# Optimization experiments

Hardware: AMD Instinct MI355X
Metric: run time of the kernel (lower is better)

Reference implementation:

```python
import jax, jax.numpy as jnp
import numpy as np

N, F, HID, OUT, H = 4096, 128, 64, 16, 4
ALPHA = 0.2          # leaky relu slope
NEG = -9e15          # mask fill value (pyGAT convention)


def setup_inputs() -> dict:
    key = jax.random.key(0)
    ks = jax.random.split(key, 8)
    x = jax.random.normal(ks[0], (N, F), dtype=jnp.float32)
    adj = jax.random.randint(ks[1], (N, N), 0, 2, dtype=jnp.int32)
    s = lambda *sh: 0.1
    W_in = jax.random.normal(ks[2], (H, F, F), dtype=jnp.float32) * 0.1
    a_in = jax.random.normal(ks[3], (H, 2 * F), dtype=jnp.float32) * 0.1
    W_hid = jax.random.normal(ks[4], (H, F * H, HID), dtype=jnp.float32) * 0.1
    a_hid = jax.random.normal(ks[5], (H, 2 * HID), dtype=jnp.float32) * 0.1
    W_out = jax.random.normal(ks[6], (HID * H, OUT), dtype=jnp.float32) * 0.1
    a_out = jax.random.normal(ks[7], (2 * OUT,), dtype=jnp.float32) * 0.1
    return {"x": x, "adj": adj, "W_in": W_in, "a_in": a_in,
            "W_hid": W_hid, "a_hid": a_hid, "W_out": W_out, "a_out": a_out}


def _multi_head_att(x, W, a, mask):
    """Dense multi-head GAT aggregation. x:[N,Fin], W:[H,Fin,D], a:[H,2D] -> [H,N,D]."""
    D = W.shape[-1]
    h = jnp.einsum('nf,hfd->hnd', x, W)                      # [H,N,D]
    f1 = jnp.einsum('hnd,hd->hn', h, a[:, :D])               # source scores
    f2 = jnp.einsum('hnd,hd->hn', h, a[:, D:])               # target scores
    e = jax.nn.leaky_relu(f1[:, :, None] + f2[:, None, :], ALPHA)  # [H,N,N]
    e = jnp.where(mask[None, :, :], e, NEG)
    att = jax.nn.softmax(e, axis=-1)
    return jnp.einsum('hnm,hmd->hnd', att, h)                # [H,N,D]


def _concat_heads(h):
    # [H,N,D] -> [N,H*D]
    Hh, n, d = h.shape
    return jnp.transpose(h, (1, 0, 2)).reshape(n, Hh * d)


def reference(x, adj, W_in, a_in, W_hid, a_hid, W_out, a_out):
    mask = adj > 0
    # input attention block: concat=True (ELU per head), identity skip (in==out dim)
    h1 = _multi_head_att(x, W_in, a_in, mask)                # [H,N,F]
    h1 = jax.nn.elu(h1 + x[None, :, :])                      # identity residual
    h1 = _concat_heads(h1)                                   # [N,H*F]
    # hidden attention block: concat=True
    h2 = _multi_head_att(h1, W_hid, a_hid, mask)             # [H,N,HID]
    h2 = _concat_heads(jax.nn.elu(h2))                       # [N,H*HID]
    # output attention layer: single head, concat=False (no ELU inside)
    h3 = _multi_head_att(h2, W_out[None], a_out[None], mask)[0]  # [N,OUT]
    return jax.nn.log_softmax(jax.nn.elu(h3), axis=1)
```

## Files before the change

### kernel.cpp

```cpp
#include <hip/hip_runtime.h>
#include <math.h>

#define NN 4096
#define FF 128
#define HH 4
#define HIDD 64
#define OUTD 16
#define MASKW (NN / 32)
#define ALPHA 0.2f

typedef __attribute__((ext_vector_type(8))) short short8;
typedef __attribute__((ext_vector_type(4))) float f32x4;

__device__ __forceinline__ ushort f2bf(float f) {
    unsigned u = __float_as_uint(f);
    return (ushort)((u + 0x7fffu + ((u >> 16) & 1u)) >> 16);
}
__device__ __forceinline__ float bf2f(ushort u) {
    return __uint_as_float((unsigned)u << 16);
}

__global__ void pack_mask_kernel(const int* __restrict__ adj, unsigned int* __restrict__ mb) {
    int t = blockIdx.x * 256 + threadIdx.x;
    int v = adj[t] > 0;
    unsigned long long bal = __ballot(v);
    if ((threadIdx.x & 63) == 0) {
        int w = t >> 5;
        mb[w] = (unsigned int)(bal & 0xffffffffULL);
        mb[w + 1] = (unsigned int)(bal >> 32);
    }
}

__global__ void cvt_kernel(const float* __restrict__ x, ushort* __restrict__ xb) {
    int e = (blockIdx.x * 256 + threadIdx.x) * 4;
    f32x4 v = *(const f32x4*)&x[e];
    unsigned lo = (unsigned)f2bf(v[0]) | ((unsigned)f2bf(v[1]) << 16);
    unsigned hi = (unsigned)f2bf(v[2]) | ((unsigned)f2bf(v[3]) << 16);
    uint2 p; p.x = lo; p.y = hi;
    *(uint2*)&xb[e] = p;
}

__global__ void wtprep_kernel(const float* __restrict__ W_in, const float* __restrict__ W_hid,
                              const float* __restrict__ W_out,
                              ushort* __restrict__ wt1, ushort* __restrict__ wt2,
                              ushort* __restrict__ wt3) {
    int idx = blockIdx.x * 256 + threadIdx.x;
    if (idx < 65536) {
        int k = idx & 127, n = (idx >> 7) & 127, hd = idx >> 14;
        wt1[idx] = f2bf(W_in[((size_t)hd * 128 + k) * 128 + n]);
    } else if (idx < 65536 + 131072) {
        int j = idx - 65536;
        int k = j & 511, n = (j >> 9) & 63, hd = j >> 15;
        wt2[j] = f2bf(W_hid[((size_t)hd * 512 + k) * 64 + n]);
    } else if (idx < 65536 + 131072 + 4096) {
        int j = idx - 196608;
        int k = j & 255, n = j >> 8;
        wt3[j] = f2bf(W_out[(size_t)k * 16 + n]);
    }
}

__global__ void vprep_kernel(const float* __restrict__ W_in, const float* __restrict__ a_in,
                             const float* __restrict__ W_hid, const float* __restrict__ a_hid,
                             const float* __restrict__ W_out, const float* __restrict__ a_out,
                             float* __restrict__ vbuf) {
    int idx = blockIdx.x * 256 + threadIdx.x;
    const float* Wr; const float* ar; int D; float* dst;
    if (idx < 1024) {
        int f = idx & 127, hd = (idx >> 7) & 3, s = idx >> 9;
        Wr = W_in + ((size_t)hd * 128 + f) * 128;
        ar = a_in + hd * 256 + s * 128;
        D = 128; dst = &vbuf[idx];
    } else if (idx < 1024 + 4096) {
        int j = idx - 1024;
        int f = j & 511, hd = (j >> 9) & 3, s = j >> 11;
        Wr = W_hid + ((size_t)hd * 512 + f) * 64;
        ar = a_hid + hd * 128 + s * 64;
        D = 64; dst = &vbuf[1024 + j];
    } else if (idx < 1024 + 4096 + 512) {
        int j = idx - 5120;
        int f = j & 255, s = j >> 8;
        Wr = W_out + (size_t)f * 16;
        ar = a_out + s * 16;
        D = 16; dst = &vbuf[5120 + j];
    } else return;
    float s = 0.f;
    for (int d = 0; d < D; d++) s += Wr[d] * ar[d];
    *dst = s;
}

template <typename T, int K, int H>
__global__ __launch_bounds__(256) void score_kernel(const T* __restrict__ A,
                                                    const float* __restrict__ v,
                                                    float* __restrict__ f1,
                                                    float* __restrict__ f2) {
    int wv = blockIdx.x * 4 + (threadIdx.x >> 6);
    int lane = threadIdx.x & 63;
    int hd = wv >> 12;
    int i = wv & (NN - 1);
    const T* ar = A + (size_t)i * K;
    const float* v1r = v + (size_t)hd * K;
    const float* v2r = v + (size_t)(H + hd) * K;
    float s1 = 0.f, s2 = 0.f;
    for (int f = lane; f < K; f += 64) {
        float av;
        if constexpr (sizeof(T) == 2) av = bf2f(((const ushort*)ar)[f]);
        else av = ((const float*)ar)[f];
        s1 += av * v1r[f];
        s2 += av * v2r[f];
    }
#pragma unroll
    for (int o = 32; o > 0; o >>= 1) {
        s1 += __shfl_down(s1, o);
        s2 += __shfl_down(s2, o);
    }
    if (lane == 0) { f1[wv] = s1; f2[wv] = s2; }
}

__global__ void gmax_kernel(const float* __restrict__ f2, float* __restrict__ gmax) {
    int hd = blockIdx.x;
    const float* p = f2 + (size_t)hd * NN;
    float m = -1e30f;
    for (int i = threadIdx.x; i < NN; i += 256) m = fmaxf(m, p[i]);
    __shared__ float sm[4];
#pragma unroll
    for (int off = 32; off > 0; off >>= 1) m = fmaxf(m, __shfl_down(m, off));
    if ((threadIdx.x & 63) == 0) sm[threadIdx.x >> 6] = m;
    __syncthreads();
    if (threadIdx.x == 0) gmax[hd] = fmaxf(fmaxf(sm[0], sm[1]), fmaxf(sm[2], sm[3]));
}

template <int K, int N, int CFG>
__global__ __launch_bounds__(256) void proj_mfma_kernel(const ushort* __restrict__ A,
                                                        const ushort* __restrict__ WT,
                                                        ushort* __restrict__ hT) {
    constexpr int NT = (CFG == 0) ? (N / 64) : (N / 16);
    __shared__ ushort ts[4][NT * 16][20];
    const int hd = blockIdx.y;
    const int t = threadIdx.x;
    const int w = t >> 6, lane = t & 63, ln = lane & 15, g = lane >> 4, g8 = g * 8;
    const int i0 = (CFG == 0) ? blockIdx.x * 16 : blockIdx.x * 64 + w * 16;
    const int n0 = (CFG == 0) ? w * (N / 4) : 0;
    const ushort* WTh = WT + (size_t)hd * N * K;
    ushort* hTh = hT + (size_t)hd * N * NN;
    f32x4 acc[NT];
#pragma unroll
    for (int n = 0; n < NT; n++) acc[n] = (f32x4)(0.f);
    const ushort* arow = A + (size_t)(i0 + ln) * K + g8;
#pragma unroll
    for (int k0 = 0; k0 < K; k0 += 32) {
        short8 aF = *(const short8*)&arow[k0];
#pragma unroll
        for (int n = 0; n < NT; n++) {
            short8 bF = *(const short8*)&WTh[(size_t)(n0 + n * 16 + ln) * K + k0 + g8];
            acc[n] = __builtin_amdgcn_mfma_f32_16x16x32_bf16(aF, bF, acc[n], 0, 0, 0);
        }
    }
#pragma unroll
    for (int n = 0; n < NT; n++) {
        unsigned lo = (unsigned)f2bf(acc[n][0]) | ((unsigned)f2bf(acc[n][1]) << 16);
        unsigned hi = (unsigned)f2bf(acc[n][2]) | ((unsigned)f2bf(acc[n][3]) << 16);
        uint2 p; p.x = lo; p.y = hi;
        *(uint2*)&ts[w][n * 16 + ln][g * 4] = p;
    }
#pragma unroll
    for (int n = 0; n < NT; n++) {
        int d = lane >> 2, ip = lane & 3;
        uint2 rv = *(uint2*)&ts[w][n * 16 + d][ip * 4];
        *(uint2*)&hTh[(size_t)(n0 + n * 16 + d) * NN + i0 + ip * 4] = rv;
    }
}

template <int D>
__global__ __launch_bounds__(256) void agg4_kernel(const ushort* __restrict__ hT,
                                                   const float* __restrict__ f1,
                                                   const float* __restrict__ f2,
                                                   const float* __restrict__ gmax,
                                                   const unsigned int* __restrict__ mb,
                                                   float* __restrict__ pacc,
                                                   float* __restrict__ plsum,
                                                   int lgJS) {
    constexpr int NT = D / 16;
    constexpr int CHS = NT * 64;
    constexpr int NC = NT / 2;
    __shared__ ushort hs[2 * CHS * 8];
    const int JS = 1 << lgJS;
    const int jlen = NN >> lgJS;
    const int combos = JS * HH;
    const int bid = blockIdx.x;
    int ibk, combo;
    if (combos >= 8) {
        int xcd = bid & 7;
        int sid = bid >> 3;
        combo = xcd * (combos >> 3) + (sid >> 6);
        ibk = sid & 63;
    } else {
        ibk = bid & 63;
        combo = bid >> 6;
    }
    const int js = combo & (JS - 1);
    const int hd = combo >> lgJS;
    const int jb = js * jlen, je = jb + jlen;

    const int t = threadIdx.x;
    const int w = t >> 6;
    const int lane = t & 63;
    const int ln = lane & 15;
    const int g = lane >> 4;
    const int g8 = g * 8;
    const int i0 = ibk * 64 + w * 16;
    const ushort* hTh = hT + (size_t)hd * D * NN;

    const float f1v = f1[hd * NN + i0 + ln];
    const float gm = gmax[hd];
    float mi = f1v + gm;
    mi = fmaxf(mi, ALPHA * mi);
    const float L2E = 1.442695040888963f;
    const float cexp = -mi * L2E;

    f32x4 acc[NT];
#pragma unroll
    for (int n = 0; n < NT; n++) acc[n] = (f32x4)(0.f);
    float lsum = 0.f;
    const float* f2h = f2 + hd * NN;
    const unsigned* mrow = mb + (size_t)(i0 + ln) * MASKW;

    int srow[NC], scol[NC], soff[NC];
#pragma unroll
    for (int c = 0; c < NC; c++) {
        int ch = t + c * 256;
        int s = ch / CHS;
        int inner = ch - s * CHS;
        int n = inner >> 6;
        int l = inner & 63;
        srow[c] = n * 16 + (l & 15);
        scol[c] = s * 32 + (l >> 4) * 8;
        soff[c] = ch * 8;
    }
    uint4 st[NC];
#pragma unroll
    for (int c = 0; c < NC; c++)
        st[c] = *(const uint4*)&hTh[(size_t)srow[c] * NN + jb + scol[c]];

    for (int j0 = jb; j0 < je; j0 += 64) {
        __syncthreads();
#pragma unroll
        for (int c = 0; c < NC; c++) *(uint4*)&hs[soff[c]] = st[c];
        __syncthreads();
        const bool more = (j0 + 64) < je;
        if (more) {
#pragma unroll
            for (int c = 0; c < NC; c++)
                st[c] = *(const uint4*)&hTh[(size_t)srow[c] * NN + j0 + 64 + scol[c]];
        }
        uint2 mw2 = *(const uint2*)&mrow[j0 >> 5];
#pragma unroll
        for (int s = 0; s < 2; s++) {
            unsigned bits = ((s ? mw2.y : mw2.x) >> g8) & 0xffu;
            f32x4 cA = *(const f32x4*)&f2h[j0 + s * 32 + g8];
            f32x4 cB = *(const f32x4*)&f2h[j0 + s * 32 + g8 + 4];
            unsigned au[4];
#pragma unroll
            for (int tp = 0; tp < 4; tp++) {
                unsigned pu[2];
#pragma unroll
                for (int q = 0; q < 2; q++) {
                    int tt = tp * 2 + q;
                    float f2t = (tt < 4) ? cA[tt] : cB[tt - 4];
                    float e = f1v + f2t;
                    e = fmaxf(e, ALPHA * e);
                    float p = ((bits >> tt) & 1u) ? __builtin_amdgcn_exp2f(e * L2E + cexp) : 0.f;
                    pu[q] = __float_as_uint(p) & 0xffff0000u;
                    lsum += __uint_as_float(pu[q]);
                }
                au[tp] = (pu[0] >> 16) | pu[1];
            }
            union { unsigned u[4]; short8 v; } aF;
#pragma unroll
            for (int q = 0; q < 4; q++) aF.u[q] = au[q];
#pragma unroll
            for (int n = 0; n < NT; n++) {
                short8 bF = *(const short8*)&hs[((s * NT + n) * 64 + lane) * 8];
                acc[n] = __builtin_amdgcn_mfma_f32_16x16x32_bf16(aF.v, bF, acc[n], 0, 0, 0);
            }
        }
    }
    lsum += __shfl_xor(lsum, 16);
    lsum += __shfl_xor(lsum, 32);
    if (g == 0) plsum[(size_t)combo * NN + i0 + ln] = lsum;
    float* pb = pacc + ((size_t)combo * NN + i0) * D;
#pragma unroll
    for (int n = 0; n < NT; n++) {
#pragma unroll
        for (int r = 0; r < 4; r++) {
            pb[n * 256 + (g * 4 + r) * 16 + ln] = acc[n][r];
        }
    }
}

template <int D, int EPI>
__global__ __launch_bounds__(256) void combine_kernel(const float* __restrict__ pacc,
                                                      const float* __restrict__ plsum,
                                                      const float* __restrict__ xres,
                                                      ushort* __restrict__ out,
                                                      int ncols, int JS) {
    const int hd = blockIdx.y;
    const int e = (blockIdx.x * 256 + threadIdx.x) * 4;
    const int row = e / D;
    const int col = e % D;
    const size_t fidx = ((size_t)(row & ~15)) * D + (col >> 4) * 256 + (row & 15) * 16 + (col & 15);
    f32x4 s = (f32x4)(0.f);
    float l = 0.f;
    for (int js = 0; js < JS; js++) {
        const size_t cix = (size_t)(hd * JS + js) * NN;
        s += *(const f32x4*)&pacc[cix * D + fidx];
        l += plsum[cix + row];
    }
    const float inv = 1.f / l;
    f32x4 xv;
    if (EPI == 1) xv = *(const f32x4*)&xres[(size_t)row * D + col];
    float o[4];
#pragma unroll
    for (int k = 0; k < 4; k++) {
        float v = s[k] * inv;
        if (EPI == 1) v += xv[k];
        if (EPI >= 1) v = v > 0.f ? v : (__expf(v) - 1.f);
        o[k] = v;
    }
    unsigned lo = (unsigned)f2bf(o[0]) | ((unsigned)f2bf(o[1]) << 16);
    unsigned hi = (unsigned)f2bf(o[2]) | ((unsigned)f2bf(o[3]) << 16);
    uint2 p; p.x = lo; p.y = hi;
    *(uint2*)&out[(size_t)row * ncols + hd * D + col] = p;
}

template <int D, int EPI>
__global__ __launch_bounds__(256) void agg2_kernel(const ushort* __restrict__ hT,
                                                   const float* __restrict__ f1,
                                                   const float* __restrict__ f2,
                                                   const float* __restrict__ gmax,
                                                   const unsigned int* __restrict__ mb,
                                                   const float* __restrict__ xres,
                                                   ushort* __restrict__ out, int ncols) {
    constexpr int NT = D / 16;
    constexpr int NC = D / 64;
    __shared__ ushort hs[D][40];
    const int hd = blockIdx.z;
    const int t = threadIdx.x;
    const int w = t >> 6;
    const int lane = t & 63;
    const int ln = lane & 15;
    const int g = lane >> 4;
    const int g8 = g * 8;
    const int i0 = blockIdx.x * 64 + w * 16;
    const ushort* hTh = hT + (size_t)hd * D * NN;
    const float f1v = f1[hd * NN + i0 + ln];
    const float gm = gmax[hd];
    float mi = f1v + gm;
    mi = fmaxf(mi, ALPHA * mi);
    const float L2E = 1.442695040888963f;
    const float cexp = -mi * L2E;
    f32x4 acc[NT];
#pragma unroll
    for (int n = 0; n < NT; n++) acc[n] = (f32x4)(0.f);
    float lsum = 0.f;
    const float* f2h = f2 + hd * NN;
    const unsigned* mrow = mb + (size_t)(i0 + ln) * MASKW;
    int srow[NC], scol[NC];
#pragma unroll
    for (int c = 0; c < NC; c++) {
        int ch = t + c * 256;
        srow[c] = ch >> 2;
        scol[c] = (ch & 3) * 8;
    }
    uint4 st[NC];
#pragma unroll
    for (int c = 0; c < NC; c++)
        st[c] = *(const uint4*)&hTh[(size_t)srow[c] * NN + scol[c]];
    unsigned mw = mrow[0];
    f32x4 fA = *(const f32x4*)&f2h[g8];
    f32x4 fB = *(const f32x4*)&f2h[g8 + 4];
    for (int j0 = 0; j0 < NN; j0 += 32) {
        __syncthreads();
#pragma unroll
        for (int c = 0; c < NC; c++) *(uint4*)&hs[srow[c]][scol[c]] = st[c];
        __syncthreads();
        const bool more = (j0 + 32) < NN;
        if (more) {
#pragma unroll
            for (int c = 0; c < NC; c++)
                st[c] = *(const uint4*)&hTh[(size_t)srow[c] * NN + j0 + 32 + scol[c]];
        }
        unsigned bits = (mw >> g8) & 0xffu;
        f32x4 cA = fA, cB = fB;
        if (more) {
            mw = mrow[(j0 + 32) >> 5];
            fA = *(const f32x4*)&f2h[j0 + 32 + g8];
            fB = *(const f32x4*)&f2h[j0 + 32 + g8 + 4];
        }
        unsigned au[4];
#pragma unroll
        for (int tp = 0; tp < 4; tp++) {
            unsigned pu[2];
#pragma unroll
            for (int q = 0; q < 2; q++) {
                int tt = tp * 2 + q;
                float f2t = (tt < 4) ? cA[tt] : cB[tt - 4];
                float e = f1v + f2t;
                e = fmaxf(e, ALPHA * e);
                float p = ((bits >> tt) & 1u) ? __builtin_amdgcn_exp2f(e * L2E + cexp) : 0.f;
                pu[q] = __float_as_uint(p) & 0xffff0000u;
                lsum += __uint_as_float(pu[q]);
            }
            au[tp] = (pu[0] >> 16) | pu[1];
        }
        union { unsigned u[4]; short8 s; } aF;
#pragma unroll
        for (int q = 0; q < 4; q++) aF.u[q] = au[q];
#pragma unroll
        for (int n = 0; n < NT; n++) {
            short8 bF = *(const short8*)&hs[n * 16 + ln][g8];
            acc[n] = __builtin_amdgcn_mfma_f32_16x16x32_bf16(aF.s, bF, acc[n], 0, 0, 0);
        }
    }
    lsum += __shfl_xor(lsum, 16);
    lsum += __shfl_xor(lsum, 32);
    const float linv = 1.f / lsum;
#pragma unroll
    for (int n = 0; n < NT; n++) {
#pragma unroll
        for (int r = 0; r < 4; r++) {
            float invr = __shfl(linv, (g << 2) + r);
            float v = acc[n][r] * invr;
            int row = i0 + g * 4 + r;
            int col = n * 16 + ln;
            if (EPI == 1) v += xres[(size_t)row * D + col];
            if (EPI >= 1) v = v > 0.f ? v : (__expf(v) - 1.f);
            out[(size_t)row * ncols + hd * D + col] = f2bf(v);
        }
    }
}

template <int D, int EPI, int NW>
__global__ __launch_bounds__(NW * 64) void agg_mfma_kernel(const ushort* __restrict__ hT,
                                                           const float* __restrict__ f1,
                                                           const float* __restrict__ f2,
                                                           const float* __restrict__ gmax,
                                                           const unsigned int* __restrict__ mb,
                                                           const float* __restrict__ xres,
                                                           float* __restrict__ out, int ncols) {
    constexpr int NT = D / 16;
    static_assert(NW == 1 || NT == 1, "j-split only for single-tile D");
    const int hd = blockIdx.z;
    const int i0 = blockIdx.x * 16;
    const int w = threadIdx.x >> 6;
    const int lane = threadIdx.x & 63;
    const int ln = lane & 15;
    const int g = lane >> 4;
    const int g8 = g * 8;
    const ushort* hTh = hT + (size_t)hd * D * NN;
    const float f1v = f1[hd * NN + i0 + ln];
    const float gm = gmax[hd];
    float mi = f1v + gm;
    mi = fmaxf(mi, ALPHA * mi);
    f32x4 acc[NT];
#pragma unroll
    for (int n = 0; n < NT; n++) acc[n] = (f32x4)(0.f);
    float lsum = 0.f;
    const float* f2h = f2 + hd * NN;
    const unsigned* mrow = mb + (size_t)(i0 + ln) * MASKW;
    const int jbeg = w * (NN / NW), jend = jbeg + NN / NW;

    for (int j0 = jbeg; j0 < jend; j0 += 32) {
        unsigned bits = (mrow[j0 >> 5] >> g8) & 0xffu;
        f32x4 fA = *(const f32x4*)&f2h[j0 + g8];
        f32x4 fB = *(const f32x4*)&f2h[j0 + g8 + 4];
        short8 aF;
#pragma unroll
        for (int t = 0; t < 8; t++) {
            float f2t = (t < 4) ? fA[t] : fB[t - 4];
            float e = f1v + f2t;
            e = fmaxf(e, ALPHA * e);
            float p = ((bits >> t) & 1u) ? __expf(e - mi) : 0.f;
            ushort pb = f2bf(p);
            aF[t] = (short)pb;
            lsum += __uint_as_float((unsigned)pb << 16);
        }
#pragma unroll
        for (int n = 0; n < NT; n++) {
            short8 bF = *(const short8*)&hTh[(size_t)(n * 16 + ln) * NN + j0 + g8];
            acc[n] = __builtin_amdgcn_mfma_f32_16x16x32_bf16(aF, bF, acc[n], 0, 0, 0);
        }
    }
    lsum += __shfl_xor(lsum, 16);
    lsum += __shfl_xor(lsum, 32);

    float accF[NT][4];
    float ltot;
    __shared__ float accL[NW][16][17];
    __shared__ float lsL[NW][16];
    if constexpr (NW == 1) {
#pragma unroll
        for (int n = 0; n < NT; n++)
#pragma unroll
            for (int r = 0; r < 4; r++) accF[n][r] = acc[n][r];
        ltot = lsum;
    } else {
#pragma unroll
        for (int r = 0; r < 4; r++) accL[w][g * 4 + r][ln] = acc[0][r];
        if (lane < 16) lsL[w][lane] = lsum;
        __syncthreads();
        if (w != 0) return;
#pragma unroll
        for (int r = 0; r < 4; r++) {
            float s = 0.f;
            for (int ww = 0; ww < NW; ww++) s += accL[ww][g * 4 + r][ln];
            accF[0][r] = s;
        }
        float s = 0.f;
        for (int ww = 0; ww < NW; ww++) s += lsL[ww][ln];
        ltot = s;
    }
    const float linv = 1.f / ltot;
#pragma unroll
    for (int n = 0; n < NT; n++) {
#pragma unroll
        for (int r = 0; r < 4; r++) {
            float invr = __shfl(linv, (g << 2) + r);
            float v = accF[n][r] * invr;
            int row = i0 + g * 4 + r;
            int col = n * 16 + ln;
            if (EPI == 1) v += xres[(size_t)row * D + col];
            if (EPI >= 1) v = v > 0.f ? v : (__expf(v) - 1.f);
            out[(size_t)row * ncols + hd * D + col] = v;
        }
    }
}

__global__ void final_kernel(const float* __restrict__ h3, float* __restrict__ out) {
    int i = blockIdx.x * 256 + threadIdx.x;
    if (i >= NN) return;
    float v[OUTD];
    float mx = -1e30f;
#pragma unroll
    for (int k = 0; k < OUTD; k++) {
        float e = h3[(size_t)i * OUTD + k];
        e = e > 0.f ? e : (__expf(e) - 1.f);
        v[k] = e;
        mx = fmaxf(mx, e);
    }
    float s = 0.f;
#pragma unroll
    for (int k = 0; k < OUTD; k++) s += __expf(v[k] - mx);
    float ls = logf(s);
#pragma unroll
    for (int k = 0; k < OUTD; k++) out[(size_t)i * OUTD + k] = v[k] - mx - ls;
}

extern "C" void kernel_launch(void* const* d_in, const int* in_sizes, int n_in,
                              void* d_out, int out_size, void* d_ws, size_t ws_size,
                              hipStream_t stream) {
    const float* x = (const float*)d_in[0];
    const int* adj = (const int*)d_in[1];
    const float* W_in = (const float*)d_in[2];
    const float* a_in = (const float*)d_in[3];
    const float* W_hid = (const float*)d_in[4];
    const float* a_hid = (const float*)d_in[5];
    const float* W_out = (const float*)d_in[6];
    const float* a_out = (const float*)d_in[7];
    float* out = (float*)d_out;

    char* w = (char*)d_ws;
    unsigned int* mb = (unsigned int*)w;  w += (size_t)NN * MASKW * 4;
    ushort* hT = (ushort*)w;              w += (size_t)HH * NN * FF * 2;
    ushort* xb16 = (ushort*)w;            w += (size_t)NN * FF * 2;
    ushort* cat1b = (ushort*)w;           w += (size_t)NN * (HH * FF) * 2;
    ushort* cat2b = (ushort*)w;           w += (size_t)NN * (HH * HIDD) * 2;
    ushort* wt1 = (ushort*)w;             w += 65536 * 2;
    ushort* wt2 = (ushort*)w;             w += 131072 * 2;
    ushort* wt3 = (ushort*)w;             w += 4096 * 2;
    float* vbuf = (float*)w;              w += 5632 * 4;
    float* f1 = (float*)w;                w += (size_t)HH * NN * 4;
    float* f2 = (float*)w;                w += (size_t)HH * NN * 4;
    float* gm = (float*)w;                w += 256;
    float* h3 = (float*)w;                w += (size_t)NN * OUTD * 4;
    size_t base_used = (size_t)(w - (char*)d_ws);

    int lgJS = -1;
    float* pacc = (float*)w;
    float* plsum = nullptr;
    {
        size_t per_js = (size_t)HH * NN * FF * 4;
        size_t ls_per_js = (size_t)HH * NN * 4;
        for (int lg = 3; lg >= 0; lg--) {
            size_t cand = (size_t)1 << lg;
            size_t need = base_used + cand * per_js + 8 * ls_per_js + 1024;
            if (ws_size >= need) { lgJS = lg; break; }
        }
        if (lgJS >= 0) plsum = (float*)((char*)pacc + ((size_t)1 << lgJS) * per_js);
    }
    const int JS = (lgJS >= 0) ? (1 << lgJS) : 0;
    const int lgJS2 = (lgJS >= 3) ? 3 : lgJS + 1;
    const int JS2 = 1 << lgJS2;

    hipLaunchKernelGGL(pack_mask_kernel, dim3(NN * NN / 256), dim3(256), 0, stream, adj, mb);
    hipLaunchKernelGGL(cvt_kernel, dim3(NN * FF / 1024), dim3(256), 0, stream, x, xb16);
    hipLaunchKernelGGL(wtprep_kernel, dim3(784), dim3(256), 0, stream,
                       W_in, W_hid, W_out, wt1, wt2, wt3);
    hipLaunchKernelGGL(vprep_kernel, dim3(22), dim3(256), 0, stream,
                       W_in, a_in, W_hid, a_hid, W_out, a_out, vbuf);

    hipLaunchKernelGGL((proj_mfma_kernel<FF, FF, 0>), dim3(NN / 16, HH), dim3(256), 0, stream,
                       xb16, wt1, hT);
    hipLaunchKernelGGL((score_kernel<float, FF, HH>), dim3(HH * NN / 4), dim3(256), 0, stream,
                       x, vbuf, f1, f2);
    hipLaunchKernelGGL(gmax_kernel, dim3(HH), dim3(256), 0, stream, f2, gm);
    if (JS) {
        hipLaunchKernelGGL((agg4_kernel<FF>), dim3(64 * JS * HH), dim3(256), 0, stream,
                           hT, f1, f2, gm, mb, pacc, plsum, lgJS);
        hipLaunchKernelGGL((combine_kernel<FF, 1>), dim3(NN * FF / 1024, HH), dim3(256), 0, stream,
                           pacc, plsum, x, cat1b, HH * FF, JS);
    } else {
        hipLaunchKernelGGL((agg2_kernel<FF, 1>), dim3(NN / 64, 1, HH), dim3(256), 0, stream,
                           hT, f1, f2, gm, mb, x, cat1b, HH * FF);
    }

    hipLaunchKernelGGL((proj_mfma_kernel<HH * FF, HIDD, 0>), dim3(NN / 16, HH), dim3(256), 0, stream,
                       cat1b, wt2, hT);
    hipLaunchKernelGGL((score_kernel<ushort, HH * FF, HH>), dim3(HH * NN / 4), dim3(256), 0, stream,
                       cat1b, vbuf + 1024, f1, f2);
    hipLaunchKernelGGL(gmax_kernel, dim3(HH), dim3(256), 0, stream, f2, gm);
    if (JS) {
        hipLaunchKernelGGL((agg4_kernel<HIDD>), dim3(64 * JS2 * HH), dim3(256), 0, stream,
                           hT, f1, f2, gm, mb, pacc, plsum, lgJS2);
        hipLaunchKernelGGL((combine_kernel<HIDD, 2>), dim3(NN * HIDD / 1024, HH), dim3(256), 0, stream,
                           pacc, plsum, (const float*)nullptr, cat2b, HH * HIDD, JS2);
    } else {
        hipLaunchKernelGGL((agg2_kernel<HIDD, 2>), dim3(NN / 64, 1, HH), dim3(256), 0, stream,
                           hT, f1, f2, gm, mb, (const float*)nullptr, cat2b, HH * HIDD);
    }

    hipLaunchKernelGGL((proj_mfma_kernel<HH * HIDD, OUTD, 1>), dim3(NN / 64, 1), dim3(256), 0, stream,
                       cat2b, wt3, hT);
    hipLaunchKernelGGL((score_kernel<ushort, HH * HIDD, 1>), dim3(NN / 4), dim3(256), 0, stream,
                       cat2b, vbuf + 5120, f1, f2);
    hipLaunchKernelGGL(gmax_kernel, dim3(1), dim3(256), 0, stream, f2, gm);
    hipLaunchKernelGGL((agg_mfma_kernel<OUTD, 0, 4>), dim3(NN / 16, 1, 1), dim3(256), 0, stream,
                       hT, f1, f2, gm, mb, (const float*)nullptr, h3, OUTD);

    hipLaunchKernelGGL(final_kernel, dim3(NN / 256), dim3(256), 0, stream, h3, out);
}
```

Before: 409.8 us.

## Compute softmax row sums via MFMA with ones vector and simplify split-J layout

```diff
diff --git a/kernel.cpp b/kernel.cpp
--- a/kernel.cpp
+++ b/kernel.cpp
@@ -171,7 +171,7 @@
 }
 
 template <int D>
-__global__ __launch_bounds__(256) void agg4_kernel(const ushort* __restrict__ hT,
+__global__ __launch_bounds__(256) void agg6_kernel(const ushort* __restrict__ hT,
                                                    const float* __restrict__ f1,
                                                    const float* __restrict__ f2,
                                                    const float* __restrict__ gmax,
@@ -220,7 +220,11 @@
     f32x4 acc[NT];
 #pragma unroll
     for (int n = 0; n < NT; n++) acc[n] = (f32x4)(0.f);
-    float lsum = 0.f;
+    f32x4 accl = (f32x4)(0.f);
+    short8 bONE;
+#pragma unroll
+    for (int q = 0; q < 8; q++) bONE[q] = (short)0x3F80;
+
     const float* f2h = f2 + hd * NN;
     const unsigned* mrow = mb + (size_t)(i0 + ln) * MASKW;
 
@@ -270,7 +274,6 @@
                     e = fmaxf(e, ALPHA * e);
                     float p = ((bits >> tt) & 1u) ? __builtin_amdgcn_exp2f(e * L2E + cexp) : 0.f;
                     pu[q] = __float_as_uint(p) & 0xffff0000u;
-                    lsum += __uint_as_float(pu[q]);
                 }
                 au[tp] = (pu[0] >> 16) | pu[1];
             }
@@ -282,17 +285,20 @@
                 short8 bF = *(const short8*)&hs[((s * NT + n) * 64 + lane) * 8];
                 acc[n] = __builtin_amdgcn_mfma_f32_16x16x32_bf16(aF.v, bF, acc[n], 0, 0, 0);
             }
-        }
-    }
-    lsum += __shfl_xor(lsum, 16);
-    lsum += __shfl_xor(lsum, 32);
-    if (g == 0) plsum[(size_t)combo * NN + i0 + ln] = lsum;
-    float* pb = pacc + ((size_t)combo * NN + i0) * D;
+            accl = __builtin_amdgcn_mfma_f32_16x16x32_bf16(aF.v, bONE, accl, 0, 0, 0);
+        }
+    }
+    if (ln == 0) {
+#pragma unroll
+        for (int r = 0; r < 4; r++)
+            plsum[(size_t)combo * NN + i0 + g * 4 + r] = accl[r];
+    }
+    float* pb = pacc + (size_t)combo * NN * D;
 #pragma unroll
     for (int n = 0; n < NT; n++) {
 #pragma unroll
         for (int r = 0; r < 4; r++) {
-            pb[n * 256 + (g * 4 + r) * 16 + ln] = acc[n][r];
+            pb[(size_t)(i0 + g * 4 + r) * D + n * 16 + ln] = acc[n][r];
         }
     }
 }
@@ -307,12 +313,11 @@
     const int e = (blockIdx.x * 256 + threadIdx.x) * 4;
     const int row = e / D;
     const int col = e % D;
-    const size_t fidx = ((size_t)(row & ~15)) * D + (col >> 4) * 256 + (row & 15) * 16 + (col & 15);
     f32x4 s = (f32x4)(0.f);
     float l = 0.f;
     for (int js = 0; js < JS; js++) {
         const size_t cix = (size_t)(hd * JS + js) * NN;
-        s += *(const f32x4*)&pacc[cix * D + fidx];
+        s += *(const f32x4*)&pacc[(cix + row) * D + col];
         l += plsum[cix + row];
     }
     const float inv = 1.f / l;
@@ -330,113 +335,6 @@
     unsigned hi = (unsigned)f2bf(o[2]) | ((unsigned)f2bf(o[3]) << 16);
     uint2 p; p.x = lo; p.y = hi;
     *(uint2*)&out[(size_t)row * ncols + hd * D + col] = p;
-}
-
-template <int D, int EPI>
-__global__ __launch_bounds__(256) void agg2_kernel(const ushort* __restrict__ hT,
-                                                   const float* __restrict__ f1,
-                                                   const float* __restrict__ f2,
-                                                   const float* __restrict__ gmax,
-                                                   const unsigned int* __restrict__ mb,
-                                                   const float* __restrict__ xres,
-                                                   ushort* __restrict__ out, int ncols) {
-    constexpr int NT = D / 16;
-    constexpr int NC = D / 64;
-    __shared__ ushort hs[D][40];
-    const int hd = blockIdx.z;
-    const int t = threadIdx.x;
-    const int w = t >> 6;
-    const int lane = t & 63;
-    const int ln = lane & 15;
-    const int g = lane >> 4;
-    const int g8 = g * 8;
-    const int i0 = blockIdx.x * 64 + w * 16;
-    const ushort* hTh = hT + (size_t)hd * D * NN;
-    const float f1v = f1[hd * NN + i0 + ln];
-    const float gm = gmax[hd];
-    float mi = f1v + gm;
-    mi = fmaxf(mi, ALPHA * mi);
-    const float L2E = 1.442695040888963f;
-    const float cexp = -mi * L2E;
-    f32x4 acc[NT];
-#pragma unroll
-    for (int n = 0; n < NT; n++) acc[n] = (f32x4)(0.f);
-    float lsum = 0.f;
-    const float* f2h = f2 + hd * NN;
-    const unsigned* mrow = mb + (size_t)(i0 + ln) * MASKW;
-    int srow[NC], scol[NC];
-#pragma unroll
-    for (int c = 0; c < NC; c++) {
-        int ch = t + c * 256;
-        srow[c] = ch >> 2;
-        scol[c] = (ch & 3) * 8;
-    }
-    uint4 st[NC];
-#pragma unroll
-    for (int c = 0; c < NC; c++)
-        st[c] = *(const uint4*)&hTh[(size_t)srow[c] * NN + scol[c]];
-    unsigned mw = mrow[0];
-    f32x4 fA = *(const f32x4*)&f2h[g8];
-    f32x4 fB = *(const f32x4*)&f2h[g8 + 4];
-    for (int j0 = 0; j0 < NN; j0 += 32) {
-        __syncthreads();
-#pragma unroll
-        for (int c = 0; c < NC; c++) *(uint4*)&hs[srow[c]][scol[c]] = st[c];
-        __syncthreads();
-        const bool more = (j0 + 32) < NN;
-        if (more) {
-#pragma unroll
-            for (int c = 0; c < NC; c++)
-                st[c] = *(const uint4*)&hTh[(size_t)srow[c] * NN + j0 + 32 + scol[c]];
-        }
-        unsigned bits = (mw >> g8) & 0xffu;
-        f32x4 cA = fA, cB = fB;
-        if (more) {
-            mw = mrow[(j0 + 32) >> 5];
-            fA = *(const f32x4*)&f2h[j0 + 32 + g8];
-            fB = *(const f32x4*)&f2h[j0 + 32 + g8 + 4];
-        }
-        unsigned au[4];
-#pragma unroll
-        for (int tp = 0; tp < 4; tp++) {
-            unsigned pu[2];
-#pragma unroll
-            for (int q = 0; q < 2; q++) {
-                int tt = tp * 2 + q;
-                float f2t = (tt < 4) ? cA[tt] : cB[tt - 4];
-                float e = f1v + f2t;
-                e = fmaxf(e, ALPHA * e);
-                float p = ((bits >> tt) & 1u) ? __builtin_amdgcn_exp2f(e * L2E + cexp) : 0.f;
-                pu[q] = __float_as_uint(p) & 0xffff0000u;
-                lsum += __uint_as_float(pu[q]);
-            }
-            au[tp] = (pu[0] >> 16) | pu[1];
-        }
-        union { unsigned u[4]; short8 s; } aF;
-#pragma unroll
-        for (int q = 0; q < 4; q++) aF.u[q] = au[q];
-#pragma unroll
-        for (int n = 0; n < NT; n++) {
-            short8 bF = *(const short8*)&hs[n * 16 + ln][g8];
-            acc[n] = __builtin_amdgcn_mfma_f32_16x16x32_bf16(aF.s, bF, acc[n], 0, 0, 0);
-        }
-    }
-    lsum += __shfl_xor(lsum, 16);
-    lsum += __shfl_xor(lsum, 32);
-    const float linv = 1.f / lsum;
-#pragma unroll
-    for (int n = 0; n < NT; n++) {
-#pragma unroll
-        for (int r = 0; r < 4; r++) {
-            float invr = __shfl(linv, (g << 2) + r);
-            float v = acc[n][r] * invr;
-            int row = i0 + g * 4 + r;
-            int col = n * 16 + ln;
-            if (EPI == 1) v += xres[(size_t)row * D + col];
-            if (EPI >= 1) v = v > 0.f ? v : (__expf(v) - 1.f);
-            out[(size_t)row * ncols + hd * D + col] = f2bf(v);
-        }
-    }
 }
 
 template <int D, int EPI, int NW>
@@ -589,16 +487,16 @@
     float* plsum = nullptr;
     {
         size_t per_js = (size_t)HH * NN * FF * 4;
-        size_t ls_per_js = (size_t)HH * NN * 4;
-        for (int lg = 3; lg >= 0; lg--) {
+        size_t ls_bytes = (size_t)32 * NN * 4;
+        for (int lg = 2; lg >= 0; lg--) {
             size_t cand = (size_t)1 << lg;
-            size_t need = base_used + cand * per_js + 8 * ls_per_js + 1024;
+            size_t need = base_used + cand * per_js + ls_bytes + 1024;
             if (ws_size >= need) { lgJS = lg; break; }
         }
         if (lgJS >= 0) plsum = (float*)((char*)pacc + ((size_t)1 << lgJS) * per_js);
     }
-    const int JS = (lgJS >= 0) ? (1 << lgJS) : 0;
-    const int lgJS2 = (lgJS >= 3) ? 3 : lgJS + 1;
+    const int JS = (lgJS >= 0) ? (1 << lgJS) : 1;
+    const int lgJS2 = (lgJS >= 0) ? lgJS + 1 : 0;
     const int JS2 = 1 << lgJS2;
 
     hipLaunchKernelGGL(pack_mask_kernel, dim3(NN * NN / 256), dim3(256), 0, stream, adj, mb);
@@ -613,30 +511,20 @@
     hipLaunchKernelGGL((score_kernel<float, FF, HH>), dim3(HH * NN / 4), dim3(256), 0, stream,
                        x, vbuf, f1, f2);
     hipLaunchKernelGGL(gmax_kernel, dim3(HH), dim3(256), 0, stream, f2, gm);
-    if (JS) {
-        hipLaunchKernelGGL((agg4_kernel<FF>), dim3(64 * JS * HH), dim3(256), 0, stream,
-                           hT, f1, f2, gm, mb, pacc, plsum, lgJS);
-        hipLaunchKernelGGL((combine_kernel<FF, 1>), dim3(NN * FF / 1024, HH), dim3(256), 0, stream,
-                           pacc, plsum, x, cat1b, HH * FF, JS);
-    } else {
-        hipLaunchKernelGGL((agg2_kernel<FF, 1>), dim3(NN / 64, 1, HH), dim3(256), 0, stream,
-                           hT, f1, f2, gm, mb, x, cat1b, HH * FF);
-    }
+    hipLaunchKernelGGL((agg6_kernel<FF>), dim3(64 * JS * HH), dim3(256), 0, stream,
+                       hT, f1, f2, gm, mb, pacc, plsum, lgJS < 0 ? 0 : lgJS);
+    hipLaunchKernelGGL((combine_kernel<FF, 1>), dim3(NN * FF / 1024, HH), dim3(256), 0, stream,
+                       pacc, plsum, x, cat1b, HH * FF, JS);
 
     hipLaunchKernelGGL((proj_mfma_kernel<HH * FF, HIDD, 0>), dim3(NN / 16, HH), dim3(256), 0, stream,
                        cat1b, wt2, hT);
     hipLaunchKernelGGL((score_kernel<ushort, HH * FF, HH>), dim3(HH * NN / 4), dim3(256), 0, stream,
                        cat1b, vbuf + 1024, f1, f2);
     hipLaunchKernelGGL(gmax_kernel, dim3(HH), dim3(256), 0, stream, f2, gm);
-    if (JS) {
-        hipLaunchKernelGGL((agg4_kernel<HIDD>), dim3(64 * JS2 * HH), dim3(256), 0, stream,
-                           hT, f1, f2, gm, mb, pacc, plsum, lgJS2);
-        hipLaunchKernelGGL((combine_kernel<HIDD, 2>), dim3(NN * HIDD / 1024, HH), dim3(256), 0, stream,
-                           pacc, plsum, (const float*)nullptr, cat2b, HH * HIDD, JS2);
-    } else {
-        hipLaunchKernelGGL((agg2_kernel<HIDD, 2>), dim3(NN / 64, 1, HH), dim3(256), 0, stream,
-                           hT, f1, f2, gm, mb, (const float*)nullptr, cat2b, HH * HIDD);
-    }
+    hipLaunchKernelGGL((agg6_kernel<HIDD>), dim3(64 * JS2 * HH), dim3(256), 0, stream,
+                       hT, f1, f2, gm, mb, pacc, plsum, lgJS2);
+    hipLaunchKernelGGL((combine_kernel<HIDD, 2>), dim3(NN * HIDD / 1024, HH), dim3(256), 0, stream,
+                       pacc, plsum, (const float*)nullptr, cat2b, HH * HIDD, JS2);
 
     hipLaunchKernelGGL((proj_mfma_kernel<HH * HIDD, OUTD, 1>), dim3(NN / 64, 1), dim3(256), 0, stream,
                        cat2b, wt3, hT);
```

After: 407.0 us. About the same (-0.7%).
